# Kernel tuning notes

Measured on AMD Instinct MI355X. Metric: run time of the kernel, lower is better.

## Reference

```python
import jax, jax.numpy as jnp
import numpy as np

B, S = 1, 2048
HID, INTER = 4096, 11008
HEADS, HD = 32, 128
GS = 128
EPS = 1e-6
BASE = 10000.0
IMIN, IMAX = -(2**31), 2**31 - 1


def _rope_tables():
    inv_freq = 1.0 / (BASE ** (np.arange(0, HD, 2, dtype=np.float32) / HD))
    t = np.arange(S, dtype=np.float32)
    freqs = np.outer(t, inv_freq)            # [S, HD/2]
    emb = np.concatenate([freqs, freqs], -1)  # [S, HD]
    return jnp.asarray(np.sin(emb), jnp.float32), jnp.asarray(np.cos(emb), jnp.float32)


def setup_inputs() -> dict:
    key = jax.random.key(0)
    ks = iter(jax.random.split(key, 40))
    def qset(in_f, out_f):
        qw = jax.random.randint(next(ks), (in_f // 8, out_f), IMIN, IMAX, dtype=jnp.int32)
        qz = jax.random.randint(next(ks), (in_f // GS, out_f // 8), IMIN, IMAX, dtype=jnp.int32)
        sc = jax.random.uniform(next(ks), (in_f // GS, out_f), dtype=jnp.float32) * 0.01 + 1e-3
        return qw, qz, sc
    dims = {"q": (HID, HID), "k": (HID, HID), "v": (HID, HID), "o": (HID, HID),
            "gate": (HID, INTER), "up": (HID, INTER), "down": (INTER, HID)}
    inp = {}
    for name, (i, o) in dims.items():
        qw, qz, sc = qset(i, o)
        inp["qw_" + name] = qw
        inp["qz_" + name] = qz
        inp["sc_" + name] = sc
    inp["hidden_states"] = jax.random.normal(next(ks), (B, S, HID), dtype=jnp.float32)
    inp["ln1_w"] = jnp.ones((HID,), jnp.float32)
    inp["ln2_w"] = jnp.ones((HID,), jnp.float32)
    sin, cos = _rope_tables()
    inp["sin"] = sin
    inp["cos"] = cos
    # causal additive mask, as stored in ExLlamaBuffer.attn_mask (past_len = 0)
    mask = jnp.where(jnp.tril(jnp.ones((S, S), bool)), 0.0, -1e9).astype(jnp.float32)
    inp["attn_mask"] = mask[None, None]
    return inp


def _dequant(qw, qz, sc):
    # GPTQ int4: qweight [in/8, out] packs 8 rows per int32; qzeros [groups, out/8]
    in_f, out_f = qw.shape[0] * 8, qw.shape[1]
    groups = sc.shape[0]
    sh = jnp.arange(8, dtype=jnp.int32) * 4
    w = ((qw[:, None, :] >> sh[None, :, None]) & 15)
    w = w.reshape(groups, in_f // groups, out_f).astype(jnp.float32)
    z = ((qz[:, :, None] >> sh[None, None, :]) & 15).reshape(groups, out_f).astype(jnp.float32)
    return ((w - (z + 1.0)[:, None, :]) * sc[:, None, :]).reshape(in_f, out_f)


def _rms(x, w):
    v = jnp.mean(x * x, axis=-1, keepdims=True)
    return x * jax.lax.rsqrt(v + EPS) * w


def _rot_half(x):
    x1, x2 = jnp.split(x, 2, axis=-1)
    return jnp.concatenate([-x2, x1], axis=-1)


def reference(qw_q, qz_q, sc_q, qw_k, qz_k, sc_k, qw_v, qz_v, sc_v,
              qw_o, qz_o, sc_o, qw_gate, qz_gate, sc_gate,
              qw_up, qz_up, sc_up, qw_down, qz_down, sc_down,
              hidden_states, ln1_w, ln2_w, sin, cos, attn_mask):
    lin = lambda x, a, b, c: x @ _dequant(a, b, c)
    h = hidden_states
    # attention block
    x = _rms(h, ln1_w)
    q = lin(x, qw_q, qz_q, sc_q).reshape(B, S, HEADS, HD).transpose(0, 2, 1, 3)
    k = lin(x, qw_k, qz_k, sc_k).reshape(B, S, HEADS, HD).transpose(0, 2, 1, 3)
    v = lin(x, qw_v, qz_v, sc_v).reshape(B, S, HEADS, HD).transpose(0, 2, 1, 3)
    c, s = cos[None, None], sin[None, None]  # [1,1,S,HD]
    q = q * c + _rot_half(q) * s
    k = k * c + _rot_half(k) * s
    scores = jnp.einsum('bhqd,bhkd->bhqk', q, k) / np.float32(np.sqrt(HD)) + attn_mask
    p = jax.nn.softmax(scores, axis=-1)
    o = jnp.einsum('bhqk,bhkd->bhqd', p, v).transpose(0, 2, 1, 3).reshape(B, S, HID)
    h = h + lin(o, qw_o, qz_o, sc_o)
    # MLP block
    x = _rms(h, ln2_w)
    y = jax.nn.silu(lin(x, qw_gate, qz_gate, sc_gate)) * lin(x, qw_up, qz_up, sc_up)
    return h + lin(y, qw_down, qz_down, sc_down)
```

## Files before the change

kernel.cpp:

```cpp
#include <hip/hip_runtime.h>
#include <cstdint>
#include <cstddef>

#define S_LEN 2048
#define HID   4096
#define INTER 11008
#define NHEADS 32
#define HD    128

typedef __attribute__((ext_vector_type(4))) float  f32x4;
typedef __attribute__((ext_vector_type(8))) __bf16 bf16x8;
typedef __attribute__((ext_vector_type(8))) short  s16x8;
typedef __attribute__((ext_vector_type(4))) short  s16x4;

__device__ __forceinline__ float bf2f(short s) {
  unsigned u = ((unsigned)(unsigned short)s) << 16;
  return __builtin_bit_cast(float, u);
}
__device__ __forceinline__ short f2bf(float f) {
  unsigned u = __builtin_bit_cast(unsigned, f);
  u += 0x7FFFu + ((u >> 16) & 1u);
  return (short)(u >> 16);
}
__device__ __forceinline__ f32x4 mfma16(s16x8 a, s16x8 b, f32x4 c) {
  return __builtin_amdgcn_mfma_f32_16x16x32_bf16(
      __builtin_bit_cast(bf16x8, a), __builtin_bit_cast(bf16x8, b), c, 0, 0, 0);
}
__device__ __forceinline__ void gload_lds16(const void* g, void* l) {
  __builtin_amdgcn_global_load_lds(
      (const __attribute__((address_space(1))) void*)g,
      (__attribute__((address_space(3))) void*)l, 16, 0, 0);
}

__global__ __launch_bounds__(256) void rmsnorm_kernel(const float* __restrict__ x,
                                                      const float* __restrict__ w,
                                                      short* __restrict__ out) {
  int row = blockIdx.x;
  const float* xr = x + (size_t)row * HID;
  short* orow = out + (size_t)row * HID;
  int tid = threadIdx.x;
  f32x4 v[4];
  float ss = 0.f;
#pragma unroll
  for (int i = 0; i < 4; ++i) {
    v[i] = ((const f32x4*)xr)[i * 256 + tid];
    ss += v[i][0] * v[i][0] + v[i][1] * v[i][1] + v[i][2] * v[i][2] + v[i][3] * v[i][3];
  }
#pragma unroll
  for (int off = 32; off > 0; off >>= 1) ss += __shfl_xor(ss, off);
  __shared__ float psum[4];
  if ((tid & 63) == 0) psum[tid >> 6] = ss;
  __syncthreads();
  float tot = psum[0] + psum[1] + psum[2] + psum[3];
  float r = rsqrtf(tot * (1.0f / (float)HID) + 1e-6f);
#pragma unroll
  for (int i = 0; i < 4; ++i) {
    int base = (i * 256 + tid) * 4;
    s16x4 o;
#pragma unroll
    for (int j = 0; j < 4; ++j) o[j] = f2bf(v[i][j] * r * w[base + j]);
    *(s16x4*)&orow[base] = o;
  }
}

template <int OMODE>
__global__ __launch_bounds__(256) void dqgemm_kernel(
    const short* __restrict__ A, int lda,
    const int* __restrict__ qw, const int* __restrict__ qz,
    const float* __restrict__ sc, int N,
    void* __restrict__ Cv, int ldc,
    const float* __restrict__ base, int Kext, int gnx) {
  __shared__ short As[2][128 * 32];
  __shared__ short Bs[2][4 * 128 * 8];
  int tid = threadIdx.x;
  int lane = tid & 63, wv = tid >> 6;
  int wr = wv >> 1, wc = wv & 1;
  int gtot = gnx * 16;
  int bid = blockIdx.x;
  int swz = (bid & 7) * (gtot >> 3) + (bid >> 3);
  int bn = swz % gnx, bm = swz / gnx;
  f32x4 acc[4][4] = {};
  int nk = Kext >> 5;
  int lr = lane >> 2, lc = lane & 3;
  const short* Abase = A + (size_t)(bm * 128) * lda;
  int ncol0 = bn * 128;

  auto stageA = [&](int buf, int t) {
    int k0 = t << 5;
#pragma unroll
    for (int i = 0; i < 2; ++i) {
      int r = i * 64 + wv * 16 + lr;
      gload_lds16(Abase + (size_t)r * lda + k0 + lc * 8, &As[buf][i * 2048 + wv * 512]);
    }
  };
  auto stageB = [&](int buf, int t) {
    int k0 = t << 5;
    int qrow0 = k0 >> 3;
    int g = k0 >> 7;
#pragma unroll
    for (int i = 0; i < 2; ++i) {
      int idx = tid + i * 256;
      int r = idx >> 7;
      int col = idx & 127;
      int gc = ncol0 + col;
      unsigned q = (unsigned)qw[(size_t)(qrow0 + r) * N + gc];
      float s = sc[(size_t)g * N + gc];
      unsigned zq = (unsigned)qz[(size_t)g * (N >> 3) + (gc >> 3)];
      float zs = ((float)((zq >> ((gc & 7) * 4)) & 15u) + 1.0f) * s;
      s16x8 o;
#pragma unroll
      for (int j = 0; j < 8; ++j)
        o[j] = f2bf(fmaf((float)((q >> (4 * j)) & 15u), s, -zs));
      *(s16x8*)&Bs[buf][(r * 128 + col) * 8] = o;
    }
  };
  auto compute = [&](int buf) {
    int kc = lane >> 4;
    int ra = wr * 64 + (lane & 15);
    s16x8 af[4], bfr[4];
#pragma unroll
    for (int m = 0; m < 4; ++m)
      af[m] = *(const s16x8*)&As[buf][(ra + m * 16) * 32 + kc * 8];
#pragma unroll
    for (int n = 0; n < 4; ++n)
      bfr[n] = *(const s16x8*)&Bs[buf][(kc * 128 + wc * 64 + n * 16 + (lane & 15)) * 8];
#pragma unroll
    for (int m = 0; m < 4; ++m)
#pragma unroll
      for (int n = 0; n < 4; ++n) acc[m][n] = mfma16(af[m], bfr[n], acc[m][n]);
  };

  stageA(0, 0); stageB(0, 0);
  __syncthreads();
  for (int t = 0; t < nk; ++t) {
    if (t + 1 < nk) { stageA((t + 1) & 1, t + 1); stageB((t + 1) & 1, t + 1); }
    compute(t & 1);
    __syncthreads();
  }

  int row0 = bm * 128 + wr * 64 + ((lane >> 4) << 2);
  int col0 = ncol0 + wc * 64 + (lane & 15);
#pragma unroll
  for (int m = 0; m < 4; ++m)
#pragma unroll
    for (int n = 0; n < 4; ++n)
#pragma unroll
      for (int j = 0; j < 4; ++j) {
        size_t idx = (size_t)(row0 + m * 16 + j) * ldc + col0 + n * 16;
        float a = acc[m][n][j];
        if (OMODE == 0)      ((short*)Cv)[idx] = f2bf(a);
        else if (OMODE == 1) ((float*)Cv)[idx] = base[idx] + a;
        else if (OMODE == 2) ((float*)Cv)[idx] = ((float*)Cv)[idx] + a;
        else {
          short* C = (short*)Cv;
          float g = bf2f(C[idx]);
          C[idx] = f2bf(g / (1.f + __expf(-g)) * a);
        }
      }
}

__global__ __launch_bounds__(128) void rope_kernel(short* __restrict__ q, short* __restrict__ k,
                                                   const float* __restrict__ sp,
                                                   const float* __restrict__ cp) {
  int s = blockIdx.x, h = blockIdx.y;
  short* p = (blockIdx.z ? k : q) + (size_t)s * HID + h * HD;
  int d = threadIdx.x;
  float x = bf2f(p[d]);
  float xp = bf2f(p[d ^ 64]);
  float rot = (d < 64) ? -xp : xp;
  float y = x * cp[s * HD + d] + rot * sp[s * HD + d];
  __syncthreads();
  p[d] = f2bf(y);
}

__global__ __launch_bounds__(256, 2) void attn_kernel(const short* __restrict__ qb,
                                                      const short* __restrict__ kb,
                                                      const short* __restrict__ vb,
                                                      short* __restrict__ ob) {
  int qt = (int)(gridDim.x - 1) - blockIdx.x;
  int h = blockIdx.y;
  int tid = threadIdx.x, lane = tid & 63, wv = tid >> 6;
  __shared__ short Kl[64 * 128];
  __shared__ short Vl[128 * 72];
  __shared__ short Pl[4][32 * 72];
  int q0 = qt * 128 + wv * 32;
  s16x8 qf[2][4];
#pragma unroll
  for (int m = 0; m < 2; ++m)
#pragma unroll
    for (int kf = 0; kf < 4; ++kf) {
      int r = q0 + m * 16 + (lane & 15);
      int d = kf * 32 + (lane >> 4) * 8;
      qf[m][kf] = *(const s16x8*)&qb[(size_t)r * HID + h * HD + d];
    }
  f32x4 o[2][8] = {};
  float mrow[2][4], lrow[2][4];
#pragma unroll
  for (int m = 0; m < 2; ++m)
#pragma unroll
    for (int j = 0; j < 4; ++j) { mrow[m][j] = -1e30f; lrow[m][j] = 0.f; }

  auto load_tile = [&](int kv0, s16x8* kr, s16x8* vr) {
#pragma unroll
    for (int i = 0; i < 4; ++i) {
      int cid = tid + i * 256;
      int kv = cid >> 4, c = cid & 15;
      kr[i] = *(const s16x8*)(kb + (size_t)(kv0 + kv) * HID + h * HD + c * 8);
      vr[i] = *(const s16x8*)(vb + (size_t)(kv0 + kv) * HID + h * HD + c * 8);
    }
  };
  auto store_tile = [&](const s16x8* kr, const s16x8* vr) {
#pragma unroll
    for (int i = 0; i < 4; ++i) {
      int cid = tid + i * 256;
      int kv = cid >> 4, c = cid & 15;
      *(s16x8*)((char*)Kl + kv * 256 + ((c ^ (kv & 7)) * 16)) = kr[i];
      int kvs = kv ^ ((c & 7) << 3);
#pragma unroll
      for (int j = 0; j < 8; ++j) Vl[(c * 8 + j) * 72 + kvs] = vr[i][j];
    }
  };

  const float scale = 0.08838834764831845f;
  int kv_end = qt * 128 + 128;
  s16x8 kra[4], vra[4], krb[4], vrb[4];
  load_tile(0, kra, vra);
  store_tile(kra, vra);
  __syncthreads();
  for (int kv0 = 0; kv0 < kv_end; kv0 += 64) {
    bool more = kv0 + 64 < kv_end;
    if (more) load_tile(kv0 + 64, krb, vrb);

    f32x4 sfr[2][4] = {};
    __builtin_amdgcn_s_setprio(1);
#pragma unroll
    for (int nf = 0; nf < 4; ++nf) {
      s16x8 kfr[4];
      int kvr = nf * 16 + (lane & 15);
#pragma unroll
      for (int kf = 0; kf < 4; ++kf) {
        int cc = (kf * 4 + (lane >> 4)) ^ (kvr & 7);
        kfr[kf] = *(const s16x8*)((const char*)Kl + kvr * 256 + cc * 16);
      }
#pragma unroll
      for (int m = 0; m < 2; ++m)
#pragma unroll
        for (int kf = 0; kf < 4; ++kf) sfr[m][nf] = mfma16(qf[m][kf], kfr[kf], sfr[m][nf]);
    }
    __builtin_amdgcn_s_setprio(0);
#pragma unroll
    for (int m = 0; m < 2; ++m)
#pragma unroll
      for (int j = 0; j < 4; ++j) {
        int qrow = q0 + m * 16 + (lane >> 4) * 4 + j;
        float pm = -1e30f;
#pragma unroll
        for (int nf = 0; nf < 4; ++nf) {
          int kvc = kv0 + nf * 16 + (lane & 15);
          float v = sfr[m][nf][j] * scale;
          v = (kvc <= qrow) ? v : -1e30f;
          sfr[m][nf][j] = v;
          pm = fmaxf(pm, v);
        }
#pragma unroll
        for (int off = 1; off < 16; off <<= 1) pm = fmaxf(pm, __shfl_xor(pm, off));
        float mnew = fmaxf(mrow[m][j], pm);
        float alpha = __expf(mrow[m][j] - mnew);
        mrow[m][j] = mnew;
        float rs = 0.f;
#pragma unroll
        for (int nf = 0; nf < 4; ++nf) {
          float pv = __expf(sfr[m][nf][j] - mnew);
          sfr[m][nf][j] = pv;
          rs += pv;
        }
#pragma unroll
        for (int off = 1; off < 16; off <<= 1) rs += __shfl_xor(rs, off);
        lrow[m][j] = lrow[m][j] * alpha + rs;
#pragma unroll
        for (int nd = 0; nd < 8; ++nd) o[m][nd][j] *= alpha;
      }
#pragma unroll
    for (int m = 0; m < 2; ++m)
#pragma unroll
      for (int nf = 0; nf < 4; ++nf)
#pragma unroll
        for (int j = 0; j < 4; ++j)
          Pl[wv][(m * 16 + (lane >> 4) * 4 + j) * 72 + nf * 16 + (lane & 15)] =
              f2bf(sfr[m][nf][j]);
    s16x8 pa[2][2];
#pragma unroll
    for (int m = 0; m < 2; ++m)
#pragma unroll
      for (int kf = 0; kf < 2; ++kf)
        pa[m][kf] = *(const s16x8*)&Pl[wv][(m * 16 + (lane & 15)) * 72 + kf * 32 + (lane >> 4) * 8];
    __builtin_amdgcn_s_setprio(1);
#pragma unroll
    for (int nd = 0; nd < 8; ++nd) {
      s16x8 vf[2];
      int drow = nd * 16 + (lane & 15);
      int key = ((drow >> 3) & 7) << 3;
#pragma unroll
      for (int kf = 0; kf < 2; ++kf)
        vf[kf] = *(const s16x8*)&Vl[drow * 72 + ((kf * 32 + (lane >> 4) * 8) ^ key)];
#pragma unroll
      for (int m = 0; m < 2; ++m)
#pragma unroll
        for (int kf = 0; kf < 2; ++kf) o[m][nd] = mfma16(pa[m][kf], vf[kf], o[m][nd]);
    }
    __builtin_amdgcn_s_setprio(0);
    __syncthreads();
    if (more) store_tile(krb, vrb);
    __syncthreads();
  }
#pragma unroll
  for (int m = 0; m < 2; ++m)
#pragma unroll
    for (int nd = 0; nd < 8; ++nd)
#pragma unroll
      for (int j = 0; j < 4; ++j) {
        int r = q0 + m * 16 + (lane >> 4) * 4 + j;
        int c = h * HD + nd * 16 + (lane & 15);
        ob[(size_t)r * HID + c] = f2bf(o[m][nd][j] / lrow[m][j]);
      }
}

extern "C" void kernel_launch(void* const* d_in, const int* in_sizes, int n_in,
                              void* d_out, int out_size, void* d_ws, size_t ws_size,
                              hipStream_t stream) {
  const int* qw[7]; const int* qz[7]; const float* sc[7];
  for (int i = 0; i < 7; ++i) {
    qw[i] = (const int*)d_in[i * 3 + 0];
    qz[i] = (const int*)d_in[i * 3 + 1];
    sc[i] = (const float*)d_in[i * 3 + 2];
  }
  const float* hin  = (const float*)d_in[21];
  const float* ln1  = (const float*)d_in[22];
  const float* ln2  = (const float*)d_in[23];
  const float* sinp = (const float*)d_in[24];
  const float* cosp = (const float*)d_in[25];
  float* out = (float*)d_out;

  char* ws = (char*)d_ws;
  const size_t MB = 1024 * 1024;
  short* XB = (short*)(ws);
  short* QB = (short*)(ws + 16 * MB);
  short* KB = (short*)(ws + 32 * MB);
  short* VB = (short*)(ws + 48 * MB);
  short* OB = (short*)(ws + 64 * MB);
  short* YB = (short*)(ws + 80 * MB);

  dim3 blk(256);

  rmsnorm_kernel<<<S_LEN, blk, 0, stream>>>(hin, ln1, XB);
  dqgemm_kernel<0><<<512, blk, 0, stream>>>(XB, HID, qw[0], qz[0], sc[0], HID, QB, HID, nullptr, HID, 32);
  dqgemm_kernel<0><<<512, blk, 0, stream>>>(XB, HID, qw[1], qz[1], sc[1], HID, KB, HID, nullptr, HID, 32);
  dqgemm_kernel<0><<<512, blk, 0, stream>>>(XB, HID, qw[2], qz[2], sc[2], HID, VB, HID, nullptr, HID, 32);
  rope_kernel<<<dim3(S_LEN, NHEADS, 2), dim3(128), 0, stream>>>(QB, KB, sinp, cosp);
  attn_kernel<<<dim3(S_LEN / 128, NHEADS), blk, 0, stream>>>(QB, KB, VB, OB);
  dqgemm_kernel<1><<<512, blk, 0, stream>>>(OB, HID, qw[3], qz[3], sc[3], HID, out, HID, hin, HID, 32);
  rmsnorm_kernel<<<S_LEN, blk, 0, stream>>>(out, ln2, XB);
  dqgemm_kernel<0><<<1376, blk, 0, stream>>>(XB, HID, qw[4], qz[4], sc[4], INTER, YB, INTER, nullptr, HID, 86);
  dqgemm_kernel<3><<<1376, blk, 0, stream>>>(XB, HID, qw[5], qz[5], sc[5], INTER, YB, INTER, nullptr, HID, 86);
  dqgemm_kernel<2><<<512, blk, 0, stream>>>(YB, INTER, qw[6], qz[6], sc[6], HID, out, HID, nullptr, INTER, 32);
}
```

Baseline: 1.642 ms.

## Switch to fp16 MFMA with magic-number dequant and 256-row GEMM tiles

All intermediates and MFMAs move from bf16 to fp16. The int4 dequant now uses the 0x6400 magic-number trick with packed half2 subtract and multiply instead of per-element float conversion. The GEMM block grows to 512 threads covering a 256x128 tile, and the global loads of packed weights are issued two iterations ahead in registers. Together these cut dequant ALU cost and raise reuse of each dequantized B tile, at the cost of fp16 range risk and larger per-block shared memory.

New measurement: 1.491 ms. -9.2%, faster.

```diff
diff --git a/kernel.cpp b/kernel.cpp
--- a/kernel.cpp
+++ b/kernel.cpp
@@ -8,23 +8,22 @@
 #define NHEADS 32
 #define HD    128
 
-typedef __attribute__((ext_vector_type(4))) float  f32x4;
-typedef __attribute__((ext_vector_type(8))) __bf16 bf16x8;
-typedef __attribute__((ext_vector_type(8))) short  s16x8;
-typedef __attribute__((ext_vector_type(4))) short  s16x4;
-
-__device__ __forceinline__ float bf2f(short s) {
-  unsigned u = ((unsigned)(unsigned short)s) << 16;
-  return __builtin_bit_cast(float, u);
-}
-__device__ __forceinline__ short f2bf(float f) {
-  unsigned u = __builtin_bit_cast(unsigned, f);
-  u += 0x7FFFu + ((u >> 16) & 1u);
-  return (short)(u >> 16);
-}
-__device__ __forceinline__ f32x4 mfma16(s16x8 a, s16x8 b, f32x4 c) {
-  return __builtin_amdgcn_mfma_f32_16x16x32_bf16(
-      __builtin_bit_cast(bf16x8, a), __builtin_bit_cast(bf16x8, b), c, 0, 0, 0);
+typedef __attribute__((ext_vector_type(4))) float    f32x4;
+typedef __attribute__((ext_vector_type(8))) _Float16 f16x8;
+typedef __attribute__((ext_vector_type(2))) _Float16 h2;
+typedef __attribute__((ext_vector_type(8))) short    s16x8;
+typedef __attribute__((ext_vector_type(4))) short    s16x4;
+typedef __attribute__((ext_vector_type(4))) unsigned u32x4;
+
+__device__ __forceinline__ float h2f(short s) {
+  return (float)__builtin_bit_cast(_Float16, s);
+}
+__device__ __forceinline__ short f2h(float f) {
+  return __builtin_bit_cast(short, (_Float16)f);
+}
+__device__ __forceinline__ f32x4 mfma16f(s16x8 a, s16x8 b, f32x4 c) {
+  return __builtin_amdgcn_mfma_f32_16x16x32_f16(
+      __builtin_bit_cast(f16x8, a), __builtin_bit_cast(f16x8, b), c, 0, 0, 0);
 }
 __device__ __forceinline__ void gload_lds16(const void* g, void* l) {
   __builtin_amdgcn_global_load_lds(
@@ -58,87 +57,98 @@
     int base = (i * 256 + tid) * 4;
     s16x4 o;
 #pragma unroll
-    for (int j = 0; j < 4; ++j) o[j] = f2bf(v[i][j] * r * w[base + j]);
+    for (int j = 0; j < 4; ++j) o[j] = f2h(v[i][j] * r * w[base + j]);
     *(s16x4*)&orow[base] = o;
   }
 }
 
 template <int OMODE>
-__global__ __launch_bounds__(256) void dqgemm_kernel(
+__global__ __launch_bounds__(512) void dqgemm_kernel(
     const short* __restrict__ A, int lda,
     const int* __restrict__ qw, const int* __restrict__ qz,
     const float* __restrict__ sc, int N,
     void* __restrict__ Cv, int ldc,
     const float* __restrict__ base, int Kext, int gnx) {
-  __shared__ short As[2][128 * 32];
+  __shared__ short As[2][256 * 32];
   __shared__ short Bs[2][4 * 128 * 8];
   int tid = threadIdx.x;
-  int lane = tid & 63, wv = tid >> 6;
-  int wr = wv >> 1, wc = wv & 1;
-  int gtot = gnx * 16;
+  int lane = tid & 63, wid = tid >> 6;
+  int wr = wid >> 1, wc = wid & 1;
+  int gtot = gnx * 8;
   int bid = blockIdx.x;
   int swz = (bid & 7) * (gtot >> 3) + (bid >> 3);
   int bn = swz % gnx, bm = swz / gnx;
   f32x4 acc[4][4] = {};
   int nk = Kext >> 5;
   int lr = lane >> 2, lc = lane & 3;
-  const short* Abase = A + (size_t)(bm * 128) * lda;
+  const short* Abase = A + (size_t)(bm * 256) * lda;
   int ncol0 = bn * 128;
-
+  int bcol = tid & 127, brow = tid >> 7;
+  int gc = ncol0 + bcol;
+
+  unsigned qn = 0, znv = 0; float snv = 0.f;
+  auto ldB = [&](int t) {
+    if (t >= nk) return;
+    qn  = (unsigned)qw[(size_t)(t * 4 + brow) * N + gc];
+    snv = sc[(size_t)(t >> 2) * N + gc];
+    znv = (unsigned)qz[(size_t)(t >> 2) * (N >> 3) + (gc >> 3)];
+  };
+  auto dqB = [&](int buf) {
+    int z = (znv >> ((gc & 7) * 4)) & 15;
+    _Float16 hz = (_Float16)(float)(1025 + z);
+    _Float16 hs = (_Float16)snv;
+    h2 zc = {hz, hz}, s2 = {hs, hs};
+    u32x4 ov;
+#pragma unroll
+    for (int i = 0; i < 4; ++i) {
+      unsigned u = qn >> (8 * i);
+      unsigned pb = (u & 0xFu) | ((u & 0xF0u) << 12) | 0x64006400u;
+      h2 w = __builtin_bit_cast(h2, pb);
+      h2 r = (w - zc) * s2;
+      ov[i] = __builtin_bit_cast(unsigned, r);
+    }
+    *(u32x4*)&Bs[buf][(brow * 128 + bcol) * 8] = ov;
+  };
   auto stageA = [&](int buf, int t) {
+    if (t >= nk) return;
     int k0 = t << 5;
 #pragma unroll
     for (int i = 0; i < 2; ++i) {
-      int r = i * 64 + wv * 16 + lr;
-      gload_lds16(Abase + (size_t)r * lda + k0 + lc * 8, &As[buf][i * 2048 + wv * 512]);
-    }
-  };
-  auto stageB = [&](int buf, int t) {
-    int k0 = t << 5;
-    int qrow0 = k0 >> 3;
-    int g = k0 >> 7;
-#pragma unroll
-    for (int i = 0; i < 2; ++i) {
-      int idx = tid + i * 256;
-      int r = idx >> 7;
-      int col = idx & 127;
-      int gc = ncol0 + col;
-      unsigned q = (unsigned)qw[(size_t)(qrow0 + r) * N + gc];
-      float s = sc[(size_t)g * N + gc];
-      unsigned zq = (unsigned)qz[(size_t)g * (N >> 3) + (gc >> 3)];
-      float zs = ((float)((zq >> ((gc & 7) * 4)) & 15u) + 1.0f) * s;
-      s16x8 o;
-#pragma unroll
-      for (int j = 0; j < 8; ++j)
-        o[j] = f2bf(fmaf((float)((q >> (4 * j)) & 15u), s, -zs));
-      *(s16x8*)&Bs[buf][(r * 128 + col) * 8] = o;
+      int r = i * 128 + wid * 16 + lr;
+      gload_lds16(Abase + (size_t)r * lda + k0 + lc * 8,
+                  &As[buf][(i * 128 + wid * 16) * 32]);
     }
   };
   auto compute = [&](int buf) {
     int kc = lane >> 4;
     int ra = wr * 64 + (lane & 15);
-    s16x8 af[4], bfr[4];
+    s16x8 af[4], bf[4];
 #pragma unroll
     for (int m = 0; m < 4; ++m)
       af[m] = *(const s16x8*)&As[buf][(ra + m * 16) * 32 + kc * 8];
 #pragma unroll
     for (int n = 0; n < 4; ++n)
-      bfr[n] = *(const s16x8*)&Bs[buf][(kc * 128 + wc * 64 + n * 16 + (lane & 15)) * 8];
+      bf[n] = *(const s16x8*)&Bs[buf][(kc * 128 + wc * 64 + n * 16 + (lane & 15)) * 8];
 #pragma unroll
     for (int m = 0; m < 4; ++m)
 #pragma unroll
-      for (int n = 0; n < 4; ++n) acc[m][n] = mfma16(af[m], bfr[n], acc[m][n]);
-  };
-
-  stageA(0, 0); stageB(0, 0);
+      for (int n = 0; n < 4; ++n) acc[m][n] = mfma16f(af[m], bf[n], acc[m][n]);
+  };
+
+  ldB(0);
+  stageA(0, 0);
+  dqB(0);
+  ldB(1);
   __syncthreads();
   for (int t = 0; t < nk; ++t) {
-    if (t + 1 < nk) { stageA((t + 1) & 1, t + 1); stageB((t + 1) & 1, t + 1); }
-    compute(t & 1);
+    int cb = t & 1, nb = cb ^ 1;
+    if (t + 1 < nk) { dqB(nb); stageA(nb, t + 1); }
+    ldB(t + 2);
+    compute(cb);
     __syncthreads();
   }
 
-  int row0 = bm * 128 + wr * 64 + ((lane >> 4) << 2);
+  int row0 = bm * 256 + wr * 64 + ((lane >> 4) << 2);
   int col0 = ncol0 + wc * 64 + (lane & 15);
 #pragma unroll
   for (int m = 0; m < 4; ++m)
@@ -148,13 +158,13 @@
       for (int j = 0; j < 4; ++j) {
         size_t idx = (size_t)(row0 + m * 16 + j) * ldc + col0 + n * 16;
         float a = acc[m][n][j];
-        if (OMODE == 0)      ((short*)Cv)[idx] = f2bf(a);
+        if (OMODE == 0)      ((short*)Cv)[idx] = f2h(a);
         else if (OMODE == 1) ((float*)Cv)[idx] = base[idx] + a;
         else if (OMODE == 2) ((float*)Cv)[idx] = ((float*)Cv)[idx] + a;
         else {
           short* C = (short*)Cv;
-          float g = bf2f(C[idx]);
-          C[idx] = f2bf(g / (1.f + __expf(-g)) * a);
+          float g = h2f(C[idx]);
+          C[idx] = f2h(g / (1.f + __expf(-g)) * a);
         }
       }
 }
@@ -165,12 +175,12 @@
   int s = blockIdx.x, h = blockIdx.y;
   short* p = (blockIdx.z ? k : q) + (size_t)s * HID + h * HD;
   int d = threadIdx.x;
-  float x = bf2f(p[d]);
-  float xp = bf2f(p[d ^ 64]);
+  float x = h2f(p[d]);
+  float xp = h2f(p[d ^ 64]);
   float rot = (d < 64) ? -xp : xp;
   float y = x * cp[s * HD + d] + rot * sp[s * HD + d];
   __syncthreads();
-  p[d] = f2bf(y);
+  p[d] = f2h(y);
 }
 
 __global__ __launch_bounds__(256, 2) void attn_kernel(const short* __restrict__ qb,
@@ -245,7 +255,7 @@
 #pragma unroll
       for (int m = 0; m < 2; ++m)
 #pragma unroll
-        for (int kf = 0; kf < 4; ++kf) sfr[m][nf] = mfma16(qf[m][kf], kfr[kf], sfr[m][nf]);
+        for (int kf = 0; kf < 4; ++kf) sfr[m][nf] = mfma16f(qf[m][kf], kfr[kf], sfr[m][nf]);
     }
     __builtin_amdgcn_s_setprio(0);
 #pragma unroll
@@ -287,7 +297,7 @@
 #pragma unroll
         for (int j = 0; j < 4; ++j)
           Pl[wv][(m * 16 + (lane >> 4) * 4 + j) * 72 + nf * 16 + (lane & 15)] =
-              f2bf(sfr[m][nf][j]);
+              f2h(sfr[m][nf][j]);
     s16x8 pa[2][2];
 #pragma unroll
     for (int m = 0; m < 2; ++m)
@@ -306,7 +316,7 @@
 #pragma unroll
       for (int m = 0; m < 2; ++m)
 #pragma unroll
-        for (int kf = 0; kf < 2; ++kf) o[m][nd] = mfma16(pa[m][kf], vf[kf], o[m][nd]);
+        for (int kf = 0; kf < 2; ++kf) o[m][nd] = mfma16f(pa[m][kf], vf[kf], o[m][nd]);
     }
     __builtin_amdgcn_s_setprio(0);
     __syncthreads();
@@ -321,7 +331,7 @@
       for (int j = 0; j < 4; ++j) {
         int r = q0 + m * 16 + (lane >> 4) * 4 + j;
         int c = h * HD + nd * 16 + (lane & 15);
-        ob[(size_t)r * HID + c] = f2bf(o[m][nd][j] / lrow[m][j]);
+        ob[(size_t)r * HID + c] = f2h(o[m][nd][j] / lrow[m][j]);
       }
 }
 
@@ -350,17 +360,17 @@
   short* OB = (short*)(ws + 64 * MB);
   short* YB = (short*)(ws + 80 * MB);
 
-  dim3 blk(256);
-
-  rmsnorm_kernel<<<S_LEN, blk, 0, stream>>>(hin, ln1, XB);
-  dqgemm_kernel<0><<<512, blk, 0, stream>>>(XB, HID, qw[0], qz[0], sc[0], HID, QB, HID, nullptr, HID, 32);
-  dqgemm_kernel<0><<<512, blk, 0, stream>>>(XB, HID, qw[1], qz[1], sc[1], HID, KB, HID, nullptr, HID, 32);
-  dqgemm_kernel<0><<<512, blk, 0, stream>>>(XB, HID, qw[2], qz[2], sc[2], HID, VB, HID, nullptr, HID, 32);
+  dim3 b256(256), b512(512);
+
+  rmsnorm_kernel<<<S_LEN, b256, 0, stream>>>(hin, ln1, XB);
+  dqgemm_kernel<0><<<256, b512, 0, stream>>>(XB, HID, qw[0], qz[0], sc[0], HID, QB, HID, nullptr, HID, 32);
+  dqgemm_kernel<0><<<256, b512, 0, stream>>>(XB, HID, qw[1], qz[1], sc[1], HID, KB, HID, nullptr, HID, 32);
+  dqgemm_kernel<0><<<256, b512, 0, stream>>>(XB, HID, qw[2], qz[2], sc[2], HID, VB, HID, nullptr, HID, 32);
   rope_kernel<<<dim3(S_LEN, NHEADS, 2), dim3(128), 0, stream>>>(QB, KB, sinp, cosp);
-  attn_kernel<<<dim3(S_LEN / 128, NHEADS), blk, 0, stream>>>(QB, KB, VB, OB);
-  dqgemm_kernel<1><<<512, blk, 0, stream>>>(OB, HID, qw[3], qz[3], sc[3], HID, out, HID, hin, HID, 32);
-  rmsnorm_kernel<<<S_LEN, blk, 0, stream>>>(out, ln2, XB);
-  dqgemm_kernel<0><<<1376, blk, 0, stream>>>(XB, HID, qw[4], qz[4], sc[4], INTER, YB, INTER, nullptr, HID, 86);
-  dqgemm_kernel<3><<<1376, blk, 0, stream>>>(XB, HID, qw[5], qz[5], sc[5], INTER, YB, INTER, nullptr, HID, 86);
-  dqgemm_kernel<2><<<512, blk, 0, stream>>>(YB, INTER, qw[6], qz[6], sc[6], HID, out, HID, nullptr, INTER, 32);
-}
+  attn_kernel<<<dim3(S_LEN / 128, NHEADS), b256, 0, stream>>>(QB, KB, VB, OB);
+  dqgemm_kernel<1><<<256, b512, 0, stream>>>(OB, HID, qw[3], qz[3], sc[3], HID, out, HID, hin, HID, 32);
+  rmsnorm_kernel<<<S_LEN, b256, 0, stream>>>(out, ln2, XB);
+  dqgemm_kernel<0><<<688, b512, 0, stream>>>(XB, HID, qw[4], qz[4], sc[4], INTER, YB, INTER, nullptr, HID, 86);
+  dqgemm_kernel<3><<<688, b512, 0, stream>>>(XB, HID, qw[5], qz[5], sc[5], INTER, YB, INTER, nullptr, HID, 86);
+  dqgemm_kernel<2><<<256, b512, 0, stream>>>(YB, INTER, qw[6], qz[6], sc[6], HID, out, HID, nullptr, INTER, 32);
+}
```
